# Optimization experiments

Hardware: AMD Instinct MI355X
Metric: run time of the kernel (lower is better)

Reference implementation:

```python
import jax, jax.numpy as jnp
import numpy as np

LOOKUP_WINDOW = 101  # module init arg
EPS = 1e-12  # F.normalize eps


def setup_inputs() -> dict:
    key = jax.random.key(0)
    k1, k2, k3 = jax.random.split(key, 3)
    B, T, F_IN, D = 4, 2048, 2048, 128
    x = jax.random.normal(k1, (B, T, F_IN), dtype=jnp.float32)
    # nn.Linear(in_filters, output_dim); stored here as [in, out] so y = x @ W + b
    W = jax.random.normal(k2, (F_IN, D), dtype=jnp.float32) / np.sqrt(F_IN).astype(np.float32)
    b = jax.random.normal(k3, (D,), dtype=jnp.float32) * 0.01
    return {"x": x, "W": W, "b": b}


def reference(x, W, b):
    hw = LOOKUP_WINDOW // 2
    # projection + L2 normalize over feature dim (F.normalize p=2, dim=-1)
    p = x @ W + b  # [B,T,D]
    p = p / jnp.maximum(jnp.linalg.norm(p, axis=-1, keepdims=True), EPS)
    B, T, D = p.shape
    # zero-pad along time so out-of-range neighbors contribute 0 similarity
    pp = jnp.pad(p, ((0, 0), (hw, hw), (0, 0)))  # [B, T+2*hw, D]
    # window gather: idx[t, w] = t + w indexes padded time axis (neighbor t + w - hw)
    idx = jnp.arange(T)[:, None] + jnp.arange(LOOKUP_WINDOW)[None, :]  # [T, W]
    windows = pp[:, idx, :]  # [B, T, W, D]
    # banded similarity: sim[b,t,w] = <p[b,t], neighbor at offset w-hw>
    sim = jnp.einsum('btd,btwd->btw', p, windows)
    return sim  # [B, T, LOOKUP_WINDOW]
```

## Files before the change

kernel.cpp:

```cpp
#include <hip/hip_runtime.h>
#include <hip/hip_bf16.h>

#define T_LEN 2048
#define D_DIM 128
#define K_DIM 2048
#define M_DIM 8192
#define LOOKUP 101
#define HWIN 50

typedef __attribute__((ext_vector_type(8))) short short8;
typedef __attribute__((ext_vector_type(4))) float f32x4;

static __device__ __forceinline__ unsigned int f2bf(float f) {
  unsigned int u = __float_as_uint(f);
  return (u + 0x7fffu + ((u >> 16) & 1u)) >> 16;
}

static __device__ __forceinline__ short8 pack8(float4 lo, float4 hi) {
  uint4 u;
  u.x = f2bf(lo.x) | (f2bf(lo.y) << 16);
  u.y = f2bf(lo.z) | (f2bf(lo.w) << 16);
  u.z = f2bf(hi.x) | (f2bf(hi.y) << 16);
  u.w = f2bf(hi.z) | (f2bf(hi.w) << 16);
  return *(short8*)&u;
}

__global__ __launch_bounds__(256) void k_pack(const float* __restrict__ W,
                                              unsigned short* __restrict__ Bp) {
  __shared__ float sw[32][132];
  const int ks = blockIdx.x;
  const int t = threadIdx.x;
  const float* src = W + (size_t)ks * 32 * D_DIM;
#pragma unroll
  for (int j = 0; j < 4; ++j) {
    int idx = t + j * 256;
    int row = idx >> 5, c4 = idx & 31;
    float4 v = *(const float4*)(src + row * D_DIM + c4 * 4);
    *(float4*)&sw[row][c4 * 4] = v;
  }
  __syncthreads();
#pragma unroll
  for (int e = 0; e < 2; ++e) {
    int f = t * 2 + e;
    int ct = f >> 6, l = f & 63;
    int kr = (l >> 4) * 8, col = ct * 16 + (l & 15);
    uint4 o;
    o.x = f2bf(sw[kr + 0][col]) | (f2bf(sw[kr + 1][col]) << 16);
    o.y = f2bf(sw[kr + 2][col]) | (f2bf(sw[kr + 3][col]) << 16);
    o.z = f2bf(sw[kr + 4][col]) | (f2bf(sw[kr + 5][col]) << 16);
    o.w = f2bf(sw[kr + 6][col]) | (f2bf(sw[kr + 7][col]) << 16);
    *(uint4*)(Bp + (((size_t)(ks * 8 + ct) << 6) + l) * 8) = o;
  }
}

__global__ __launch_bounds__(512, 4) void k_gemm(const float* __restrict__ X,
                                                 const unsigned short* __restrict__ Bp,
                                                 const float* __restrict__ bias,
                                                 unsigned short* __restrict__ Pn) {
  __shared__ __align__(16) unsigned char Pw[8 * 8192];
  const int tid = threadIdx.x;
  const int lane = tid & 63;
  const int wv = tid >> 6;
  const int r0 = blockIdx.x * 16;
  const int l15 = lane & 15;
  const int kg = lane >> 4;

  const float* xb = X + (size_t)(r0 + l15) * K_DIM + wv * 256 + kg * 8;

  f32x4 acc[8];
#pragma unroll
  for (int i = 0; i < 8; ++i) acc[i] = (f32x4){0.f, 0.f, 0.f, 0.f};

  float4 xc[2];
  short8 wc[8];
  xc[0] = *(const float4*)(xb);
  xc[1] = *(const float4*)(xb + 4);
#pragma unroll
  for (int ct = 0; ct < 8; ++ct)
    wc[ct] = *(const short8*)(Bp + (((size_t)(wv * 8) * 8 + ct) * 64 + lane) * 8);

#pragma unroll
  for (int s = 0; s < 8; ++s) {
    float4 xn[2];
    short8 wn[8];
    if (s < 7) {
      xn[0] = *(const float4*)(xb + (s + 1) * 32);
      xn[1] = *(const float4*)(xb + (s + 1) * 32 + 4);
#pragma unroll
      for (int ct = 0; ct < 8; ++ct)
        wn[ct] = *(const short8*)(Bp + (((size_t)(wv * 8 + s + 1) * 8 + ct) * 64 + lane) * 8);
    }
    short8 xf = pack8(xc[0], xc[1]);
#pragma unroll
    for (int ct = 0; ct < 8; ++ct)
      acc[ct] = __builtin_amdgcn_mfma_f32_16x16x32_bf16(wc[ct], xf, acc[ct], 0, 0, 0);
    if (s < 7) {
      xc[0] = xn[0]; xc[1] = xn[1];
#pragma unroll
      for (int ct = 0; ct < 8; ++ct) wc[ct] = wn[ct];
    }
  }

  unsigned char* pwb = Pw + wv * 8192;
#pragma unroll
  for (int ct = 0; ct < 8; ++ct) {
    int byte = l15 * 512 + ((ct * 64 + kg * 16) ^ ((l15 & 7) << 4));
    *(float4*)(pwb + byte) = make_float4(acc[ct][0], acc[ct][1], acc[ct][2], acc[ct][3]);
  }
  __syncthreads();

  const int row = tid >> 5;
  const int c4 = tid & 31;
  const int rbyte = row * 512 + ((c4 * 16) ^ ((row & 7) << 4));
  float4 tot = make_float4(0.f, 0.f, 0.f, 0.f);
#pragma unroll
  for (int q = 0; q < 8; ++q) {
    float4 v = *(const float4*)(Pw + q * 8192 + rbyte);
    tot.x += v.x; tot.y += v.y; tot.z += v.z; tot.w += v.w;
  }
  float4 bv = *(const float4*)(bias + c4 * 4);
  tot.x += bv.x; tot.y += bv.y; tot.z += bv.z; tot.w += bv.w;
  float ss = tot.x * tot.x + tot.y * tot.y + tot.z * tot.z + tot.w * tot.w;
  ss += __shfl_xor(ss, 1);
  ss += __shfl_xor(ss, 2);
  ss += __shfl_xor(ss, 4);
  ss += __shfl_xor(ss, 8);
  ss += __shfl_xor(ss, 16);
  float sc = 1.0f / fmaxf(sqrtf(ss), 1e-12f);
  unsigned int p0 = f2bf(tot.x * sc) | (f2bf(tot.y * sc) << 16);
  unsigned int p1 = f2bf(tot.z * sc) | (f2bf(tot.w * sc) << 16);
  *(uint2*)(Pn + (size_t)(r0 + row) * D_DIM + c4 * 4) = make_uint2(p0, p1);
}

#define SROWS 144

__global__ __launch_bounds__(256) void k_sim(const unsigned short* __restrict__ Pn,
                                             float* __restrict__ out) {
  __shared__ unsigned short sm[SROWS * D_DIM];
  const int bb = blockIdx.x >> 6;
  const int tb = blockIdx.x & 63;
  const int t0 = tb * 32;
  const int tid = threadIdx.x;

  for (int idx = tid; idx < SROWS * 16; idx += 256) {
    int i = idx >> 4, seg = idx & 15;
    int t = t0 - HWIN + i;
    uint4 val = make_uint4(0u, 0u, 0u, 0u);
    if (t >= 0 && t < T_LEN)
      val = *(const uint4*)(Pn + ((size_t)bb * T_LEN + t) * D_DIM + seg * 8);
    *(uint4*)&sm[i * D_DIM + ((seg ^ (i & 7)) << 3)] = val;
  }
  __syncthreads();

  const int lane = tid & 63;
  const int wv = tid >> 6;
  const int l15 = lane & 15;
  const int kg = lane >> 4;
  const int rt = wv >> 1;
  const int itp = wv & 1;

  short8 af[4];
  const int ia = HWIN + rt * 16 + l15;
#pragma unroll
  for (int ks = 0; ks < 4; ++ks) {
    int g = ks * 4 + kg;
    af[ks] = *(const short8*)&sm[ia * D_DIM + ((g ^ (ia & 7)) << 3)];
  }

  for (int it = itp; it < 9; it += 2) {
    f32x4 acc = (f32x4){0.f, 0.f, 0.f, 0.f};
    const int ib = it * 16 + l15;
#pragma unroll
    for (int ks = 0; ks < 4; ++ks) {
      int g = ks * 4 + kg;
      short8 bf = *(const short8*)&sm[ib * D_DIM + ((g ^ (ib & 7)) << 3)];
      acc = __builtin_amdgcn_mfma_f32_16x16x32_bf16(af[ks], bf, acc, 0, 0, 0);
    }
#pragma unroll
    for (int j = 0; j < 4; ++j) {
      int r = rt * 16 + kg * 4 + j;
      int w = ib - r;
      if (w >= 0 && w <= 100)
        out[((size_t)bb * T_LEN + t0 + r) * LOOKUP + w] = acc[j];
    }
  }
}

extern "C" void kernel_launch(void* const* d_in, const int* in_sizes, int n_in,
                              void* d_out, int out_size, void* d_ws, size_t ws_size,
                              hipStream_t stream) {
  (void)in_sizes; (void)n_in; (void)out_size; (void)ws_size;
  const float* x = (const float*)d_in[0];
  const float* W = (const float*)d_in[1];
  const float* b = (const float*)d_in[2];
  float* out = (float*)d_out;
  unsigned short* Bp = (unsigned short*)d_ws;
  unsigned short* Pn = Bp + (size_t)D_DIM * K_DIM;

  k_pack<<<64, 256, 0, stream>>>(W, Bp);
  k_gemm<<<M_DIM / 16, 512, 0, stream>>>(x, Bp, b, Pn);
  k_sim<<<4 * (T_LEN / 32), 256, 0, stream>>>(Pn, out);
}
```

Baseline: 34.50 us.

## Process 32 rows per GEMM block to reuse W fragments across two row groups

Each GEMM block now computes 32 output rows instead of 16, so every loaded bf16 W fragment feeds two MFMA row groups and total W traffic from L2 halves. The split-K reduction is reworked so the upper four waves write partials to LDS and the lower four add theirs in place, keeping LDS at 64KB. A final pass sums the four buffers with 8 columns per thread. This doubles accumulator registers, lowers the occupancy bound, and halves the grid to 256 blocks, which may leave compute units underused.

```diff
diff --git a/kernel.cpp b/kernel.cpp
--- a/kernel.cpp
+++ b/kernel.cpp
@@ -53,83 +53,123 @@
   }
 }
 
-__global__ __launch_bounds__(512, 4) void k_gemm(const float* __restrict__ X,
+__global__ __launch_bounds__(512, 2) void k_gemm(const float* __restrict__ X,
                                                  const unsigned short* __restrict__ Bp,
                                                  const float* __restrict__ bias,
                                                  unsigned short* __restrict__ Pn) {
-  __shared__ __align__(16) unsigned char Pw[8 * 8192];
+  __shared__ __align__(16) unsigned char Pw[4 * 16384];
   const int tid = threadIdx.x;
   const int lane = tid & 63;
   const int wv = tid >> 6;
-  const int r0 = blockIdx.x * 16;
+  const int r0 = blockIdx.x * 32;
   const int l15 = lane & 15;
   const int kg = lane >> 4;
 
-  const float* xb = X + (size_t)(r0 + l15) * K_DIM + wv * 256 + kg * 8;
-
-  f32x4 acc[8];
-#pragma unroll
-  for (int i = 0; i < 8; ++i) acc[i] = (f32x4){0.f, 0.f, 0.f, 0.f};
-
-  float4 xc[2];
-  short8 wc[8];
-  xc[0] = *(const float4*)(xb);
-  xc[1] = *(const float4*)(xb + 4);
+  const float* xb0 = X + (size_t)(r0 + l15) * K_DIM + wv * 256 + kg * 8;
+  const float* xb1 = xb0 + (size_t)16 * K_DIM;
+
+  f32x4 acc[2][8];
+#pragma unroll
+  for (int g = 0; g < 2; ++g)
+#pragma unroll
+    for (int i = 0; i < 8; ++i) acc[g][i] = (f32x4){0.f, 0.f, 0.f, 0.f};
+
+  float4 xc[2][2], xn[2][2];
+  short8 wc[8], wn[8];
+
+  xc[0][0] = *(const float4*)(xb0);
+  xc[0][1] = *(const float4*)(xb0 + 4);
+  xc[1][0] = *(const float4*)(xb1);
+  xc[1][1] = *(const float4*)(xb1 + 4);
 #pragma unroll
   for (int ct = 0; ct < 8; ++ct)
     wc[ct] = *(const short8*)(Bp + (((size_t)(wv * 8) * 8 + ct) * 64 + lane) * 8);
 
 #pragma unroll
   for (int s = 0; s < 8; ++s) {
-    float4 xn[2];
-    short8 wn[8];
     if (s < 7) {
-      xn[0] = *(const float4*)(xb + (s + 1) * 32);
-      xn[1] = *(const float4*)(xb + (s + 1) * 32 + 4);
+      xn[0][0] = *(const float4*)(xb0 + (s + 1) * 32);
+      xn[0][1] = *(const float4*)(xb0 + (s + 1) * 32 + 4);
+      xn[1][0] = *(const float4*)(xb1 + (s + 1) * 32);
+      xn[1][1] = *(const float4*)(xb1 + (s + 1) * 32 + 4);
 #pragma unroll
       for (int ct = 0; ct < 8; ++ct)
         wn[ct] = *(const short8*)(Bp + (((size_t)(wv * 8 + s + 1) * 8 + ct) * 64 + lane) * 8);
     }
-    short8 xf = pack8(xc[0], xc[1]);
+    short8 xf0 = pack8(xc[0][0], xc[0][1]);
+    short8 xf1 = pack8(xc[1][0], xc[1][1]);
 #pragma unroll
     for (int ct = 0; ct < 8; ++ct)
-      acc[ct] = __builtin_amdgcn_mfma_f32_16x16x32_bf16(wc[ct], xf, acc[ct], 0, 0, 0);
+      acc[0][ct] = __builtin_amdgcn_mfma_f32_16x16x32_bf16(wc[ct], xf0, acc[0][ct], 0, 0, 0);
+#pragma unroll
+    for (int ct = 0; ct < 8; ++ct)
+      acc[1][ct] = __builtin_amdgcn_mfma_f32_16x16x32_bf16(wc[ct], xf1, acc[1][ct], 0, 0, 0);
     if (s < 7) {
-      xc[0] = xn[0]; xc[1] = xn[1];
+      xc[0][0] = xn[0][0]; xc[0][1] = xn[0][1];
+      xc[1][0] = xn[1][0]; xc[1][1] = xn[1][1];
 #pragma unroll
       for (int ct = 0; ct < 8; ++ct) wc[ct] = wn[ct];
     }
   }
 
-  unsigned char* pwb = Pw + wv * 8192;
-#pragma unroll
-  for (int ct = 0; ct < 8; ++ct) {
-    int byte = l15 * 512 + ((ct * 64 + kg * 16) ^ ((l15 & 7) << 4));
-    *(float4*)(pwb + byte) = make_float4(acc[ct][0], acc[ct][1], acc[ct][2], acc[ct][3]);
-  }
-  __syncthreads();
-
-  const int row = tid >> 5;
-  const int c4 = tid & 31;
-  const int rbyte = row * 512 + ((c4 * 16) ^ ((row & 7) << 4));
-  float4 tot = make_float4(0.f, 0.f, 0.f, 0.f);
-#pragma unroll
-  for (int q = 0; q < 8; ++q) {
-    float4 v = *(const float4*)(Pw + q * 8192 + rbyte);
-    tot.x += v.x; tot.y += v.y; tot.z += v.z; tot.w += v.w;
-  }
-  float4 bv = *(const float4*)(bias + c4 * 4);
-  tot.x += bv.x; tot.y += bv.y; tot.z += bv.z; tot.w += bv.w;
-  float ss = tot.x * tot.x + tot.y * tot.y + tot.z * tot.z + tot.w * tot.w;
+  if (wv >= 4) {
+    unsigned char* pb = Pw + (wv - 4) * 16384;
+#pragma unroll
+    for (int rg = 0; rg < 2; ++rg)
+#pragma unroll
+      for (int ct = 0; ct < 8; ++ct) {
+        int byte = (rg * 16 + l15) * 512 + ((ct * 64 + kg * 16) ^ ((l15 & 7) << 4));
+        *(float4*)(pb + byte) = make_float4(acc[rg][ct][0], acc[rg][ct][1], acc[rg][ct][2], acc[rg][ct][3]);
+      }
+  }
+  __syncthreads();
+  if (wv < 4) {
+    unsigned char* pb = Pw + wv * 16384;
+#pragma unroll
+    for (int rg = 0; rg < 2; ++rg)
+#pragma unroll
+      for (int ct = 0; ct < 8; ++ct) {
+        int byte = (rg * 16 + l15) * 512 + ((ct * 64 + kg * 16) ^ ((l15 & 7) << 4));
+        float4 v = *(float4*)(pb + byte);
+        v.x += acc[rg][ct][0]; v.y += acc[rg][ct][1];
+        v.z += acc[rg][ct][2]; v.w += acc[rg][ct][3];
+        *(float4*)(pb + byte) = v;
+      }
+  }
+  __syncthreads();
+
+  const int row = tid >> 4;
+  const int c8 = tid & 15;
+  float tot[8];
+#pragma unroll
+  for (int i = 0; i < 8; ++i) tot[i] = 0.f;
+#pragma unroll
+  for (int q = 0; q < 4; ++q)
+#pragma unroll
+    for (int h = 0; h < 2; ++h) {
+      int byte = q * 16384 + row * 512 + (((c8 * 32 + h * 16)) ^ ((row & 7) << 4));
+      float4 v = *(const float4*)(Pw + byte);
+      tot[h * 4 + 0] += v.x; tot[h * 4 + 1] += v.y;
+      tot[h * 4 + 2] += v.z; tot[h * 4 + 3] += v.w;
+    }
+  float4 bv0 = *(const float4*)(bias + c8 * 8);
+  float4 bv1 = *(const float4*)(bias + c8 * 8 + 4);
+  tot[0] += bv0.x; tot[1] += bv0.y; tot[2] += bv0.z; tot[3] += bv0.w;
+  tot[4] += bv1.x; tot[5] += bv1.y; tot[6] += bv1.z; tot[7] += bv1.w;
+  float ss = 0.f;
+#pragma unroll
+  for (int i = 0; i < 8; ++i) ss += tot[i] * tot[i];
   ss += __shfl_xor(ss, 1);
   ss += __shfl_xor(ss, 2);
   ss += __shfl_xor(ss, 4);
   ss += __shfl_xor(ss, 8);
-  ss += __shfl_xor(ss, 16);
   float sc = 1.0f / fmaxf(sqrtf(ss), 1e-12f);
-  unsigned int p0 = f2bf(tot.x * sc) | (f2bf(tot.y * sc) << 16);
-  unsigned int p1 = f2bf(tot.z * sc) | (f2bf(tot.w * sc) << 16);
-  *(uint2*)(Pn + (size_t)(r0 + row) * D_DIM + c4 * 4) = make_uint2(p0, p1);
+  uint4 o;
+  o.x = f2bf(tot[0] * sc) | (f2bf(tot[1] * sc) << 16);
+  o.y = f2bf(tot[2] * sc) | (f2bf(tot[3] * sc) << 16);
+  o.z = f2bf(tot[4] * sc) | (f2bf(tot[5] * sc) << 16);
+  o.w = f2bf(tot[6] * sc) | (f2bf(tot[7] * sc) << 16);
+  *(uint4*)(Pn + (size_t)(r0 + row) * D_DIM + c8 * 8) = o;
 }
 
 #define SROWS 144
@@ -198,6 +238,6 @@
   unsigned short* Pn = Bp + (size_t)D_DIM * K_DIM;
 
   k_pack<<<64, 256, 0, stream>>>(W, Bp);
-  k_gemm<<<M_DIM / 16, 512, 0, stream>>>(x, Bp, b, Pn);
+  k_gemm<<<M_DIM / 32, 512, 0, stream>>>(x, Bp, b, Pn);
   k_sim<<<4 * (T_LEN / 32), 256, 0, stream>>>(Pn, out);
 }
```

Result: faster. 32.91 us (-4.6%).
